# Optimization experiments

Hardware: AMD Instinct MI355X
Metric: run time of the kernel (lower is better)

## Reference

```python
import jax, jax.numpy as jnp
import numpy as np

N, E, D, S, H, L = 20000, 320000, 128, 16, 4, 64


def _ln(x, g, b):
    m = x.mean(-1, keepdims=True)
    v = jnp.mean((x - m) ** 2, -1, keepdims=True)
    return (x - m) / jnp.sqrt(v + 1e-6) * g + b


def _mlp3(x, w1, b1, g1, be1, w2, b2, g2, be2, w3, b3):
    h = jax.nn.silu(_ln(x @ w1 + b1, g1, be1))
    h = jax.nn.silu(_ln(h @ w2 + b2, g2, be2))
    return h @ w3 + b3


def _seg_softmax(a, idx, n):
    # torch_geometric.utils.softmax: per-destination-group stable softmax
    m = jax.ops.segment_max(a, idx, num_segments=n)
    m = jnp.where(jnp.isfinite(m), m, 0.0)
    e = jnp.exp(a - m[idx])
    s = jax.ops.segment_sum(e, idx, num_segments=n)
    return e / (s[idx] + 1e-16)


def setup_inputs() -> dict:
    key = jax.random.key(0)
    ks = jax.random.split(key, 32)
    rn = lambda k, sh, sc=1.0: jax.random.normal(k, sh, dtype=jnp.float32) * sc
    li = lambda k, fi, fo: rn(k, (fi, fo), 1.0 / np.sqrt(fi))
    z = lambda n_: jnp.zeros((n_,), jnp.float32)
    o = lambda n_: jnp.ones((n_,), jnp.float32)
    inp = {
        'node_in': rn(ks[0], (N, D)),
        'node_embed': rn(ks[1], (N, D)),
        'edge_sh': rn(ks[2], (E, S)),
        'edge_length_embedding': rn(ks[3], (E, L)),
        'edge_src': jax.random.randint(ks[4], (E,), 0, N, dtype=jnp.int32),
        'edge_dst': jax.random.randint(ks[5], (E,), 0, N, dtype=jnp.int32),
        'batch': jnp.zeros((N,), jnp.int32),
        'pre_lin_w': li(ks[6], 2 * D + L, D),
        'tp2_w1': li(ks[7], L, 64), 'tp2_b1': z(64),
        'tp2_w2': li(ks[8], 64, H * S), 'tp2_b2': z(H * S),
        'a_w1': li(ks[9], L, 64), 'a_b1': z(64), 'a_g1': o(64), 'a_be1': z(64),
        'a_w2': li(ks[10], 64, 64), 'a_b2': z(64), 'a_g2': o(64), 'a_be2': z(64),
        'a_w3': li(ks[11], 64, H), 'a_b3': z(H),
        'lin_w': li(ks[12], D * H, D),
        'lin_edge_w': li(ks[13], D * H, 64),
        's_w1': li(ks[14], 64, 64), 's_b1': z(64), 's_g1': o(64), 's_be1': z(64),
        's_w2': li(ks[15], 64, 64), 's_b2': z(64), 's_g2': o(64), 's_be2': z(64),
        's_w3': li(ks[16], 64, 32), 's_b3': z(32),
    }
    return inp


def reference(node_in, node_embed, edge_sh, edge_length_embedding, edge_src, edge_dst, batch,
              pre_lin_w, tp2_w1, tp2_b1, tp2_w2, tp2_b2,
              a_w1, a_b1, a_g1, a_be1, a_w2, a_b2, a_g2, a_be2, a_w3, a_b3,
              lin_w, lin_edge_w,
              s_w1, s_b1, s_g1, s_be1, s_w2, s_b2, s_g2, s_be2, s_w3, s_b3):
    e = edge_length_embedding.shape[0]
    n = node_in.shape[0]
    # gather + pre_lin
    msg = jnp.concatenate([node_in[edge_src], node_in[edge_dst], edge_length_embedding], -1) @ pre_lin_w  # [E,D]
    # EquiConv tp2: channelwise TP with radial-MLP per-edge per-(head,sh) weights
    radial = jax.nn.silu(edge_length_embedding @ tp2_w1 + tp2_b1) @ tp2_w2 + tp2_b2  # [E,H*S]
    scal = jnp.einsum('ehs,es->eh', radial.reshape(e, H, S), edge_sh)  # [E,H]
    value = msg[:, None, :] * scal[:, :, None]  # [E,H,D]
    alpha = _mlp3(edge_length_embedding, a_w1, a_b1, a_g1, a_be1, a_w2, a_b2, a_g2, a_be2, a_w3, a_b3)  # [E,H]
    edge_out = value * alpha[:, :, None]  # [E,H,D]
    edge_scalar = _mlp3(edge_out.reshape(e, -1) @ lin_edge_w,
                        s_w1, s_b1, s_g1, s_be1, s_w2, s_b2, s_g2, s_be2, s_w3, s_b3)  # [E,32]
    asm = _seg_softmax(alpha, edge_dst, n)  # [E,H]
    node_fea = jax.ops.segment_sum(value * asm[:, :, None], edge_dst, num_segments=n)  # [N,H,D]
    node_out = node_fea.reshape(n, -1) @ lin_w  # [N,D]
    return node_out, edge_scalar
```

## Files before the change

### kernel.cpp

```cpp
#include <hip/hip_runtime.h>

#define NN 20000
#define EE 320000
#define WTOT 27648

typedef unsigned short u16;
typedef unsigned int u32;
typedef __attribute__((ext_vector_type(8))) short bf16x8;
typedef __attribute__((ext_vector_type(8))) _Float16 f16x8;
typedef __attribute__((ext_vector_type(4))) float f32x4;

__device__ __forceinline__ float bf2f(u16 u){
  union { u32 i; float f; } v; v.i = ((u32)u) << 16; return v.f;
}
__device__ __forceinline__ u16 f2bf(float f){
  union { float f; u32 i; } v; v.f = f;
  u32 i = v.i;
  return (u16)((i + 0x7FFFu + ((i >> 16) & 1u)) >> 16);
}
__device__ __forceinline__ u32 pack2(float a, float b){
  return ((u32)f2bf(b) << 16) | (u32)f2bf(a);
}
__device__ __forceinline__ u16 f2h(float f){
  union { _Float16 h[2]; u32 u; } v; v.h[0] = (_Float16)f;
  return (u16)(v.u & 0xFFFF);
}

__global__ __launch_bounds__(256) void k_prep(
    const float* __restrict__ plw, const float* __restrict__ lew,
    const float* __restrict__ lw,
    u16* __restrict__ Bt1, u16* __restrict__ Bt2, u16* __restrict__ Bt3)
{
  int i = blockIdx.x * 256 + threadIdx.x;
  if (i < 128*320) {
    int n = i / 320, k = i % 320;
    Bt1[i] = f2bf(plw[k*128 + n]);
  }
  int j = i - 128*320;
  if (j >= 0 && j < 256*128) {
    int n = j / 128, k = j % 128;
    int h = n >> 6, c = n & 63;
    Bt2[j] = f2bf(lew[(h*128 + k)*64 + c]);
  }
  int l = i - 128*320 - 256*128;
  if (l >= 0 && l < 128*512) {
    int n = l / 512, k = l % 512;
    Bt3[l] = f2bf(lw[k*128 + n]);
  }
}

__global__ __launch_bounds__(256) void k_prep2(
    const float* __restrict__ aw1, const float* __restrict__ aw2, const float* __restrict__ aw3,
    const float* __restrict__ rw1, const float* __restrict__ rw2,
    const float* __restrict__ sw1, const float* __restrict__ sw2, const float* __restrict__ sw3,
    u16* __restrict__ W)
{
  int i = blockIdx.x * 256 + threadIdx.x;
  if (i >= WTOT) return;
  float v = 0.f;
  int j = i;
  if (j < 8192)      { int n = j >> 6, k = j & 63;
                       v = (n < 64) ? aw1[k*64 + n] : rw1[k*64 + (n - 64)]; }
  else if ((j -= 8192) < 4096) { int n = j >> 6, k = j & 63; v = aw2[k*64 + n]; }
  else if ((j -= 4096) < 1024) { int n = j >> 6, k = j & 63; v = (n < 4) ? aw3[k*4 + n] : 0.f; }
  else if ((j -= 1024) < 4096) { int n = j >> 6, k = j & 63; v = rw2[k*64 + n]; }
  else if ((j -= 4096) < 4096) { int n = j >> 6, k = j & 63; v = sw1[k*64 + n]; }
  else if ((j -= 4096) < 4096) { int n = j >> 6, k = j & 63; v = sw2[k*64 + n]; }
  else               { j -= 4096; int n = j >> 6, k = j & 63; v = sw3[k*32 + n]; }
  W[i] = f2h(v);
}

__global__ __launch_bounds__(256) void k_zero(int* __restrict__ counts){
  int i = blockIdx.x * 256 + threadIdx.x;
  if (i < NN) counts[i] = 0;
}
__global__ __launch_bounds__(256) void k_count(const int* __restrict__ edst, int* __restrict__ counts){
  int e = blockIdx.x * 256 + threadIdx.x;
  if (e < EE) atomicAdd(&counts[edst[e]], 1);
}
__global__ __launch_bounds__(1024) void k_scan(const int* __restrict__ counts,
                                               int* __restrict__ offs, int* __restrict__ cursor){
  __shared__ int part[1024];
  int t = threadIdx.x;
  int c0 = t * 20, c1 = c0 + 20; if (c1 > NN) c1 = NN; if (c0 > NN) c0 = NN;
  int s = 0;
  for (int i = c0; i < c1; ++i) s += counts[i];
  part[t] = s;
  __syncthreads();
  if (t == 0) {
    int run = 0;
    for (int i = 0; i < 1024; ++i) { int v = part[i]; part[i] = run; run += v; }
    offs[NN] = run;
  }
  __syncthreads();
  int run = part[t];
  for (int i = c0; i < c1; ++i) { offs[i] = run; cursor[i] = run; run += counts[i]; }
}
__global__ __launch_bounds__(256) void k_fill(const int* __restrict__ edst,
                                              int* __restrict__ cursor, int* __restrict__ eids){
  int e = blockIdx.x * 256 + threadIdx.x;
  if (e < EE) { int p = atomicAdd(&cursor[edst[e]], 1); eids[p] = e; }
}
__global__ __launch_bounds__(256) void k_sort(const int* __restrict__ offs, int* __restrict__ eids){
  int n = blockIdx.x * 256 + threadIdx.x;
  if (n >= NN) return;
  int b = offs[n], e = offs[n+1];
  for (int i = b + 1; i < e; ++i) {
    int v = eids[i]; int j = i - 1;
    while (j >= b && eids[j] > v) { eids[j+1] = eids[j]; --j; }
    eids[j+1] = v;
  }
}

template<int NI>
__device__ __forceinline__ void gemm16_lds(const u16 (*X)[72], int wrow, int lane,
                                           const u16* __restrict__ B, f32x4 acc[2][4])
{
  const int fr = lane & 15, fc = lane >> 4;
  #pragma unroll
  for (int mi = 0; mi < 2; ++mi)
    #pragma unroll
    for (int ni = 0; ni < NI; ++ni)
      acc[mi][ni] = (f32x4){0.f, 0.f, 0.f, 0.f};
  #pragma unroll
  for (int kk = 0; kk < 2; ++kk) {
    f16x8 a0 = *(const f16x8*)&X[wrow + fr][kk*32 + fc*8];
    f16x8 a1 = *(const f16x8*)&X[wrow + 16 + fr][kk*32 + fc*8];
    #pragma unroll
    for (int ni = 0; ni < NI; ++ni) {
      f16x8 b = *(const f16x8*)(B + (size_t)(ni*16 + fr)*64 + kk*32 + fc*8);
      acc[0][ni] = __builtin_amdgcn_mfma_f32_16x16x32_f16(a0, b, acc[0][ni], 0, 0, 0);
      acc[1][ni] = __builtin_amdgcn_mfma_f32_16x16x32_f16(a1, b, acc[1][ni], 0, 0, 0);
    }
  }
}

template<int NI>
__device__ __forceinline__ void gemm16_lds1(const u16 (*X)[72], int wrow, int lane,
                                            const u16* __restrict__ B, f32x4 acc[4])
{
  const int fr = lane & 15, fc = lane >> 4;
  #pragma unroll
  for (int ni = 0; ni < NI; ++ni) acc[ni] = (f32x4){0.f, 0.f, 0.f, 0.f};
  #pragma unroll
  for (int kk = 0; kk < 2; ++kk) {
    f16x8 a = *(const f16x8*)&X[wrow + fr][kk*32 + fc*8];
    #pragma unroll
    for (int ni = 0; ni < NI; ++ni) {
      f16x8 b = *(const f16x8*)(B + (size_t)(ni*16 + fr)*64 + kk*32 + fc*8);
      acc[ni] = __builtin_amdgcn_mfma_f32_16x16x32_f16(a, b, acc[ni], 0, 0, 0);
    }
  }
}

__device__ __forceinline__ void gemm32_glb8(const float* __restrict__ X, int row0, int lane,
                                            const u16* __restrict__ B, f32x4 acc[2][8])
{
  const int fr = lane & 15, fc = lane >> 4;
  #pragma unroll
  for (int mi = 0; mi < 2; ++mi)
    #pragma unroll
    for (int ni = 0; ni < 8; ++ni)
      acc[mi][ni] = (f32x4){0.f, 0.f, 0.f, 0.f};
  #pragma unroll
  for (int kk = 0; kk < 2; ++kk) {
    const float* p0 = X + (size_t)(row0 + fr)*64 + kk*32 + fc*8;
    const float* p1 = X + (size_t)(row0 + 16 + fr)*64 + kk*32 + fc*8;
    float4 v00 = ((const float4*)p0)[0], v01 = ((const float4*)p0)[1];
    float4 v10 = ((const float4*)p1)[0], v11 = ((const float4*)p1)[1];
    f16x8 a0, a1;
    a0[0]=(_Float16)v00.x; a0[1]=(_Float16)v00.y; a0[2]=(_Float16)v00.z; a0[3]=(_Float16)v00.w;
    a0[4]=(_Float16)v01.x; a0[5]=(_Float16)v01.y; a0[6]=(_Float16)v01.z; a0[7]=(_Float16)v01.w;
    a1[0]=(_Float16)v10.x; a1[1]=(_Float16)v10.y; a1[2]=(_Float16)v10.z; a1[3]=(_Float16)v10.w;
    a1[4]=(_Float16)v11.x; a1[5]=(_Float16)v11.y; a1[6]=(_Float16)v11.z; a1[7]=(_Float16)v11.w;
    #pragma unroll
    for (int ni = 0; ni < 8; ++ni) {
      f16x8 b = *(const f16x8*)(B + (size_t)(ni*16 + fr)*64 + kk*32 + fc*8);
      acc[0][ni] = __builtin_amdgcn_mfma_f32_16x16x32_f16(a0, b, acc[0][ni], 0, 0, 0);
      acc[1][ni] = __builtin_amdgcn_mfma_f32_16x16x32_f16(a1, b, acc[1][ni], 0, 0, 0);
    }
  }
}

template<bool LN>
__device__ __forceinline__ void act_store16(f32x4 acc[2][4],
    const float* __restrict__ b, const float* __restrict__ g, const float* __restrict__ be,
    u16 (*H)[72], int wrow, int lane)
{
  const int fr = lane & 15, fc = lane >> 4;
  float bv[4], gv[4], bev[4];
  #pragma unroll
  for (int ni = 0; ni < 4; ++ni) {
    bv[ni] = b[ni*16 + fr];
    if (LN) { gv[ni] = g[ni*16 + fr]; bev[ni] = be[ni*16 + fr]; }
  }
  #pragma unroll
  for (int mi = 0; mi < 2; ++mi)
    #pragma unroll
    for (int j = 0; j < 4; ++j) {
      int r = wrow + mi*16 + fc*4 + j;
      float x[4];
      #pragma unroll
      for (int ni = 0; ni < 4; ++ni) x[ni] = acc[mi][ni][j] + bv[ni];
      if (LN) {
        float s  = x[0] + x[1] + x[2] + x[3];
        float s2 = x[0]*x[0] + x[1]*x[1] + x[2]*x[2] + x[3]*x[3];
        #pragma unroll
        for (int off = 1; off < 16; off <<= 1) {
          s  += __shfl_xor(s,  off);
          s2 += __shfl_xor(s2, off);
        }
        float mu  = s * (1.f/64.f);
        float var = s2 * (1.f/64.f) - mu*mu;
        float rs  = rsqrtf(var + 1e-6f);
        #pragma unroll
        for (int ni = 0; ni < 4; ++ni) x[ni] = (x[ni] - mu)*rs*gv[ni] + bev[ni];
      }
      #pragma unroll
      for (int ni = 0; ni < 4; ++ni) {
        float y = x[ni];
        y = y / (1.f + __expf(-y));
        H[r][ni*16 + fr] = f2h(y);
      }
    }
}

template<bool LN>
__device__ __forceinline__ void act_store16_1(f32x4 acc[4],
    const float* __restrict__ b, const float* __restrict__ g, const float* __restrict__ be,
    u16 (*H)[72], int wrow, int lane)
{
  const int fr = lane & 15, fc = lane >> 4;
  float bv[4], gv[4], bev[4];
  #pragma unroll
  for (int ni = 0; ni < 4; ++ni) {
    bv[ni] = b[ni*16 + fr];
    if (LN) { gv[ni] = g[ni*16 + fr]; bev[ni] = be[ni*16 + fr]; }
  }
  #pragma unroll
  for (int j = 0; j < 4; ++j) {
    int r = wrow + fc*4 + j;
    float x[4];
    #pragma unroll
    for (int ni = 0; ni < 4; ++ni) x[ni] = acc[ni][j] + bv[ni];
    if (LN) {
      float s  = x[0] + x[1] + x[2] + x[3];
      float s2 = x[0]*x[0] + x[1]*x[1] + x[2]*x[2] + x[3]*x[3];
      #pragma unroll
      for (int off = 1; off < 16; off <<= 1) {
        s  += __shfl_xor(s,  off);
        s2 += __shfl_xor(s2, off);
      }
      float mu  = s * (1.f/64.f);
      float var = s2 * (1.f/64.f) - mu*mu;
      float rs  = rsqrtf(var + 1e-6f);
      #pragma unroll
      for (int ni = 0; ni < 4; ++ni) x[ni] = (x[ni] - mu)*rs*gv[ni] + bev[ni];
    }
    #pragma unroll
    for (int ni = 0; ni < 4; ++ni) {
      float y = x[ni];
      y = y / (1.f + __expf(-y));
      H[r][ni*16 + fr] = f2h(y);
    }
  }
}

__global__ __launch_bounds__(256, 4) void k_ar_mlp(
  const float* __restrict__ elen,
  const float* __restrict__ esh, const u16* __restrict__ Wm,
  const float* __restrict__ ab1, const float* __restrict__ ag1, const float* __restrict__ abe1,
  const float* __restrict__ ab2, const float* __restrict__ ag2, const float* __restrict__ abe2,
  const float* __restrict__ ab3,
  const float* __restrict__ tb1, const float* __restrict__ tb2,
  float* __restrict__ alpha_g, float* __restrict__ scal_g, float* __restrict__ cbuf_g)
{
  __shared__ u16 Ha[128][72], Hr[128][72];
  __shared__ float aS[128][4];
  const u16* Wc1 = Wm;
  const u16* Wa2 = Wm + 8192;
  const u16* Wa3 = Wm + 12288;
  const u16* Wr2 = Wm + 13312;
  const int tid = threadIdx.x;
  const int wave = tid >> 6, lane = tid & 63;
  const int fr = lane & 15, fc = lane >> 4;
  const int wrow = wave * 32;
  const int e0 = blockIdx.x * 128;
  {
    f32x4 acc8[2][8];
    gemm32_glb8(elen, e0 + wrow, lane, Wc1, acc8);
    float bva[4], gva[4], beva[4], bvr[4];
    #pragma unroll
    for (int ni = 0; ni < 4; ++ni) {
      bva[ni] = ab1[ni*16 + fr]; gva[ni] = ag1[ni*16 + fr]; beva[ni] = abe1[ni*16 + fr];
      bvr[ni] = tb1[ni*16 + fr];
    }
    #pragma unroll
    for (int mi = 0; mi < 2; ++mi)
      #pragma unroll
      for (int j = 0; j < 4; ++j) {
        int r = wrow + mi*16 + fc*4 + j;
        float xa[4], xr[4];
        #pragma unroll
        for (int ni = 0; ni < 4; ++ni) {
          xa[ni] = acc8[mi][ni][j] + bva[ni];
          xr[ni] = acc8[mi][ni+4][j] + bvr[ni];
        }
        float s  = xa[0] + xa[1] + xa[2] + xa[3];
        float s2 = xa[0]*xa[0] + xa[1]*xa[1] + xa[2]*xa[2] + xa[3]*xa[3];
        #pragma unroll
        for (int off = 1; off < 16; off <<= 1) {
          s  += __shfl_xor(s,  off);
          s2 += __shfl_xor(s2, off);
        }
        float mu  = s * (1.f/64.f);
        float var = s2 * (1.f/64.f) - mu*mu;
        float rs  = rsqrtf(var + 1e-6f);
        #pragma unroll
        for (int ni = 0; ni < 4; ++ni) {
          float y = (xa[ni] - mu)*rs*gva[ni] + beva[ni];
          y = y / (1.f + __expf(-y));
          Ha[r][ni*16 + fr] = f2h(y);
          float z = xr[ni];
          z = z / (1.f + __expf(-z));
          Hr[r][ni*16 + fr] = f2h(z);
        }
      }
  }
  f32x4 acc[2][4];
  gemm16_lds<4>(Ha, wrow, lane, Wa2, acc);
  act_store16<true>(acc, ab2, ag2, abe2, Ha, wrow, lane);
  gemm16_lds<1>(Ha, wrow, lane, Wa3, acc);
  {
    float bv = (fr < 4) ? ab3[fr] : 0.f;
    #pragma unroll
    for (int mi = 0; mi < 2; ++mi)
      #pragma unroll
      for (int j = 0; j < 4; ++j) {
        int r = wrow + mi*16 + fc*4 + j;
        float v = acc[mi][0][j] + bv;
        if (fr < 4) {
          alpha_g[(size_t)(e0 + r)*4 + fr] = v;
          aS[r][fr] = v;
        }
      }
  }
  gemm16_lds<4>(Hr, wrow, lane, Wr2, acc);
  {
    float bv[4];
    #pragma unroll
    for (int ni = 0; ni < 4; ++ni) bv[ni] = tb2[ni*16 + fr];
    #pragma unroll
    for (int mi = 0; mi < 2; ++mi)
      #pragma unroll
      for (int j = 0; j < 4; ++j) {
        int r = wrow + mi*16 + fc*4 + j;
        float shv = esh[(size_t)(e0 + r)*16 + fr];
        float sc[4];
        #pragma unroll
        for (int ni = 0; ni < 4; ++ni) {
          float t = (acc[mi][ni][j] + bv[ni]) * shv;
          #pragma unroll
          for (int off = 1; off < 16; off <<= 1) t += __shfl_xor(t, off);
          sc[ni] = t;
        }
        if (fr == 0) {
          float4 sv; sv.x = sc[0]; sv.y = sc[1]; sv.z = sc[2]; sv.w = sc[3];
          *(float4*)(scal_g + (size_t)(e0 + r)*4) = sv;
          float4 cv;
          cv.x = sc[0]*aS[r][0]; cv.y = sc[1]*aS[r][1];
          cv.z = sc[2]*aS[r][2]; cv.w = sc[3]*aS[r][3];
          *(float4*)(cbuf_g + (size_t)(e0 + r)*4) = cv;
        }
      }
  }
}

__global__ __launch_bounds__(256) void g1_msg(
    const float* __restrict__ node_in, const float* __restrict__ elen,
    const int* __restrict__ esrc, const int* __restrict__ edst,
    const u16* __restrict__ Bt1, u16* __restrict__ msgb)
{
  __shared__ u16 As[128][40];
  __shared__ u16 Bs[128][40];
  const int tid = threadIdx.x;
  const int e0 = blockIdx.x * 128;
  const int wave = tid >> 6, lane = tid & 63;
  const int wr = (wave >> 1) * 64, wc = (wave & 1) * 64;
  const int fr = lane & 15, fc = lane >> 4;
  f32x4 acc[4][4] = {};
  const int r = tid >> 1, half = tid & 1;
  const int e = e0 + r;
  const int s_idx = esrc[e], d_idx = edst[e];
  for (int k0 = 0; k0 < 320; k0 += 32) {
    const int kk = k0 + half * 16;
    const float* ap;
    if (kk < 128)      ap = node_in + (size_t)s_idx*128 + kk;
    else if (kk < 256) ap = node_in + (size_t)d_idx*128 + (kk - 128);
    else               ap = elen + (size_t)e*64 + (kk - 256);
    u32* asp = (u32*)&As[r][half*16];
    #pragma unroll
    for (int q = 0; q < 4; ++q) {
      float4 v = *(const float4*)(ap + q*4);
      asp[q*2]   = pack2(v.x, v.y);
      asp[q*2+1] = pack2(v.z, v.w);
    }
    const uint4* bp = (const uint4*)(Bt1 + (size_t)r*320 + kk);
    *(uint4*)&Bs[r][half*16]     = bp[0];
    *(uint4*)&Bs[r][half*16 + 8] = bp[1];
    __syncthreads();
    bf16x8 a[4], b[4];
    #pragma unroll
    for (int mi = 0; mi < 4; ++mi) a[mi] = *(const bf16x8*)&As[wr + mi*16 + fr][fc*8];
    #pragma unroll
    for (int ni = 0; ni < 4; ++ni) b[ni] = *(const bf16x8*)&Bs[wc + ni*16 + fr][fc*8];
    #pragma unroll
    for (int mi = 0; mi < 4; ++mi)
      #pragma unroll
      for (int ni = 0; ni < 4; ++ni)
        acc[mi][ni] = __builtin_amdgcn_mfma_f32_16x16x32_bf16(a[mi], b[ni], acc[mi][ni], 0, 0, 0);
    __syncthreads();
  }
  #pragma unroll
  for (int mi = 0; mi < 4; ++mi)
    #pragma unroll
    for (int j = 0; j < 4; ++j) {
      int row = wr + mi*16 + fc*4 + j;
      size_t base = (size_t)(e0 + row)*128 + wc + fr;
      #pragma unroll
      for (int ni = 0; ni < 4; ++ni)
        msgb[base + ni*16] = f2bf(acc[mi][ni][j]);
    }
}

union G2Smem {
  struct { u16 As[64][40]; u16 Bs[256][40]; } s;
  u16 X[64][72];
};
__global__ __launch_bounds__(256, 4) void g2s(
    const u16* __restrict__ msgb, const u16* __restrict__ Bt2,
    const float* __restrict__ cbuf, const u16* __restrict__ Wm,
    const float* __restrict__ b1, const float* __restrict__ g1, const float* __restrict__ be1,
    const float* __restrict__ b2, const float* __restrict__ g2, const float* __restrict__ be2,
    const float* __restrict__ b3,
    float* __restrict__ oute)
{
  __shared__ G2Smem u;
  __shared__ float cS[64][4];
  const u16* Ws1 = Wm + 17408;
  const u16* Ws2 = Wm + 21504;
  const u16* Ws3 = Wm + 25600;
  const int tid = threadIdx.x, wave = tid >> 6, lane = tid & 63;
  const int e0 = blockIdx.x * 64;
  const int fr = lane & 15, fc = lane >> 4;
  const int wrow = wave * 16;
  cS[tid >> 2][tid & 3] = cbuf[(size_t)e0*4 + tid];
  f32x4 acc[16];
  #pragma unroll
  for (int ni = 0; ni < 16; ++ni) acc[ni] = (f32x4){0.f, 0.f, 0.f, 0.f};
  for (int k0 = 0; k0 < 128; k0 += 32) {
    {
      int r = tid >> 2, q = tid & 3;
      *(uint4*)&u.s.As[r][q*8] = *(const uint4*)(msgb + (size_t)(e0 + r)*128 + k0 + q*8);
    }
    {
      const uint4* bp = (const uint4*)(Bt2 + (size_t)tid*128 + k0);
      *(uint4*)&u.s.Bs[tid][0]  = bp[0];
      *(uint4*)&u.s.Bs[tid][8]  = bp[1];
      *(uint4*)&u.s.Bs[tid][16] = bp[2];
      *(uint4*)&u.s.Bs[tid][24] = bp[3];
    }
    __syncthreads();
    bf16x8 a = *(const bf16x8*)&u.s.As[wrow + fr][fc*8];
    #pragma unroll
    for (int ni = 0; ni < 16; ++ni) {
      bf16x8 b = *(const bf16x8*)&u.s.Bs[ni*16 + fr][fc*8];
      acc[ni] = __builtin_amdgcn_mfma_f32_16x16x32_bf16(a, b, acc[ni], 0, 0, 0);
    }
    __syncthreads();
  }
  #pragma unroll
  for (int j = 0; j < 4; ++j) {
    int r = wrow + fc*4 + j;
    float c0 = cS[r][0], c1 = cS[r][1], c2 = cS[r][2], c3 = cS[r][3];
    #pragma unroll
    for (int m = 0; m < 4; ++m) {
      float y = c0*acc[m][j] + c1*acc[4+m][j] + c2*acc[8+m][j] + c3*acc[12+m][j];
      u.X[r][m*16 + fr] = f2h(y);
    }
  }
  f32x4 sa[4];
  gemm16_lds1<4>(u.X, wrow, lane, Ws1, sa);
  act_store16_1<true>(sa, b1, g1, be1, u.X, wrow, lane);
  gemm16_lds1<4>(u.X, wrow, lane, Ws2, sa);
  act_store16_1<true>(sa, b2, g2, be2, u.X, wrow, lane);
  gemm16_lds1<2>(u.X, wrow, lane, Ws3, sa);
  {
    float bv[2];
    bv[0] = b3[fr]; bv[1] = b3[16 + fr];
    #pragma unroll
    for (int j = 0; j < 4; ++j) {
      int r = wrow + fc*4 + j;
      #pragma unroll
      for (int ni = 0; ni < 2; ++ni)
        oute[(size_t)(e0 + r)*32 + ni*16 + fr] = sa[ni][j] + bv[ni];
    }
  }
}

__global__ __launch_bounds__(256) void k_node(
  const int* __restrict__ offs, const int* __restrict__ eids,
  const float* __restrict__ alpha, const float* __restrict__ scal,
  const u16* __restrict__ msgb, u16* __restrict__ nfb)
{
  const int w = threadIdx.x >> 6, lane = threadIdx.x & 63;
  const int n = blockIdx.x * 4 + w;
  const int beg = offs[n], end = offs[n+1];
  float m0=-3e38f, m1=-3e38f, m2=-3e38f, m3=-3e38f;
  for (int i = beg + lane; i < end; i += 64) {
    int eid = eids[i];
    float4 a = *(const float4*)(alpha + (size_t)eid*4);
    m0 = fmaxf(m0, a.x); m1 = fmaxf(m1, a.y);
    m2 = fmaxf(m2, a.z); m3 = fmaxf(m3, a.w);
  }
  #pragma unroll
  for (int off = 1; off < 64; off <<= 1) {
    m0 = fmaxf(m0, __shfl_xor(m0, off));
    m1 = fmaxf(m1, __shfl_xor(m1, off));
    m2 = fmaxf(m2, __shfl_xor(m2, off));
    m3 = fmaxf(m3, __shfl_xor(m3, off));
  }
  float se0=0.f, se1=0.f, se2=0.f, se3=0.f;
  float f00=0.f, f01=0.f, f10=0.f, f11=0.f, f20=0.f, f21=0.f, f30=0.f, f31=0.f;
  for (int i = beg; i < end; ++i) {
    int eid = eids[i];
    float4 a = *(const float4*)(alpha + (size_t)eid*4);
    float4 s = *(const float4*)(scal + (size_t)eid*4);
    float e0 = __expf(a.x - m0), e1 = __expf(a.y - m1);
    float e2 = __expf(a.z - m2), e3 = __expf(a.w - m3);
    se0 += e0; se1 += e1; se2 += e2; se3 += e3;
    float w0 = e0*s.x, w1 = e1*s.y, w2 = e2*s.z, w3 = e3*s.w;
    float v0 = bf2f(msgb[(size_t)eid*128 + lane]);
    float v1 = bf2f(msgb[(size_t)eid*128 + 64 + lane]);
    f00 = fmaf(w0, v0, f00); f01 = fmaf(w0, v1, f01);
    f10 = fmaf(w1, v0, f10); f11 = fmaf(w1, v1, f11);
    f20 = fmaf(w2, v0, f20); f21 = fmaf(w2, v1, f21);
    f30 = fmaf(w3, v0, f30); f31 = fmaf(w3, v1, f31);
  }
  float i0 = 1.f/(se0 + 1e-16f), i1 = 1.f/(se1 + 1e-16f);
  float i2 = 1.f/(se2 + 1e-16f), i3 = 1.f/(se3 + 1e-16f);
  size_t b = (size_t)n * 512;
  nfb[b + 0*128 + lane]      = f2bf(f00*i0);
  nfb[b + 0*128 + 64 + lane] = f2bf(f01*i0);
  nfb[b + 1*128 + lane]      = f2bf(f10*i1);
  nfb[b + 1*128 + 64 + lane] = f2bf(f11*i1);
  nfb[b + 2*128 + lane]      = f2bf(f20*i2);
  nfb[b + 2*128 + 64 + lane] = f2bf(f21*i2);
  nfb[b + 3*128 + lane]      = f2bf(f30*i3);
  nfb[b + 3*128 + 64 + lane] = f2bf(f31*i3);
}

__global__ __launch_bounds__(256) void g10_out(
    const u16* __restrict__ nfb, const u16* __restrict__ Bt3,
    float* __restrict__ out)
{
  __shared__ u16 As[128][40];
  __shared__ u16 Bs[128][40];
  const int tid = threadIdx.x;
  const int n0 = blockIdx.x * 128;
  const int wave = tid >> 6, lane = tid & 63;
  const int wr = (wave >> 1) * 64, wc = (wave & 1) * 64;
  const int fr = lane & 15, fc = lane >> 4;
  f32x4 acc[4][4] = {};
  const int r = tid >> 1, half = tid & 1;
  const int n = n0 + r;
  for (int k0 = 0; k0 < 512; k0 += 32) {
    uint4 z; z.x=0; z.y=0; z.z=0; z.w=0;
    uint4 v0 = z, v1 = z;
    if (n < NN) {
      const uint4* apv = (const uint4*)(nfb + (size_t)n*512 + k0 + half*16);
      v0 = apv[0]; v1 = apv[1];
    }
    *(uint4*)&As[r][half*16]     = v0;
    *(uint4*)&As[r][half*16 + 8] = v1;
    const uint4* bp = (const uint4*)(Bt3 + (size_t)r*512 + k0 + half*16);
    *(uint4*)&Bs[r][half*16]     = bp[0];
    *(uint4*)&Bs[r][half*16 + 8] = bp[1];
    __syncthreads();
    bf16x8 a[4], b[4];
    #pragma unroll
    for (int mi = 0; mi < 4; ++mi) a[mi] = *(const bf16x8*)&As[wr + mi*16 + fr][fc*8];
    #pragma unroll
    for (int ni = 0; ni < 4; ++ni) b[ni] = *(const bf16x8*)&Bs[wc + ni*16 + fr][fc*8];
    #pragma unroll
    for (int mi = 0; mi < 4; ++mi)
      #pragma unroll
      for (int ni = 0; ni < 4; ++ni)
        acc[mi][ni] = __builtin_amdgcn_mfma_f32_16x16x32_bf16(a[mi], b[ni], acc[mi][ni], 0, 0, 0);
    __syncthreads();
  }
  #pragma unroll
  for (int mi = 0; mi < 4; ++mi)
    #pragma unroll
    for (int j = 0; j < 4; ++j) {
      int rowg = n0 + wr + mi*16 + fc*4 + j;
      if (rowg < NN) {
        size_t base = (size_t)rowg*128 + wc + fr;
        #pragma unroll
        for (int ni = 0; ni < 4; ++ni)
          out[base + ni*16] = acc[mi][ni][j];
      }
    }
}

extern "C" void kernel_launch(void* const* d_in, const int* in_sizes, int n_in,
                              void* d_out, int out_size, void* d_ws, size_t ws_size,
                              hipStream_t stream)
{
  const float* node_in    = (const float*)d_in[0];
  const float* edge_sh    = (const float*)d_in[2];
  const float* elen       = (const float*)d_in[3];
  const int*   esrc       = (const int*)d_in[4];
  const int*   edst       = (const int*)d_in[5];
  const float* pre_lin_w  = (const float*)d_in[7];
  const float* tp2_w1     = (const float*)d_in[8];
  const float* tp2_b1     = (const float*)d_in[9];
  const float* tp2_w2     = (const float*)d_in[10];
  const float* tp2_b2     = (const float*)d_in[11];
  const float* a_w1  = (const float*)d_in[12];
  const float* a_b1  = (const float*)d_in[13];
  const float* a_g1  = (const float*)d_in[14];
  const float* a_be1 = (const float*)d_in[15];
  const float* a_w2  = (const float*)d_in[16];
  const float* a_b2  = (const float*)d_in[17];
  const float* a_g2  = (const float*)d_in[18];
  const float* a_be2 = (const float*)d_in[19];
  const float* a_w3  = (const float*)d_in[20];
  const float* a_b3  = (const float*)d_in[21];
  const float* lin_w      = (const float*)d_in[22];
  const float* lin_edge_w = (const float*)d_in[23];
  const float* s_w1  = (const float*)d_in[24];
  const float* s_b1  = (const float*)d_in[25];
  const float* s_g1  = (const float*)d_in[26];
  const float* s_be1 = (const float*)d_in[27];
  const float* s_w2  = (const float*)d_in[28];
  const float* s_b2  = (const float*)d_in[29];
  const float* s_g2  = (const float*)d_in[30];
  const float* s_be2 = (const float*)d_in[31];
  const float* s_w3  = (const float*)d_in[32];
  const float* s_b3  = (const float*)d_in[33];

  float* out_node = (float*)d_out;
  float* out_edge = out_node + (size_t)NN * 128;

  char* ws = (char*)d_ws;
  size_t off = 0;
  auto take = [&](size_t bytes) -> char* {
    char* p = ws + off;
    off = (off + bytes + 255) & ~(size_t)255;
    return p;
  };
  u16*   msgb   = (u16*)take((size_t)EE * 128 * 2);
  u16*   nfb    = (u16*)take((size_t)NN * 512 * 2);
  float* alpha  = (float*)take((size_t)EE * 4 * 4);
  float* scal   = (float*)take((size_t)EE * 4 * 4);
  float* cbuf   = (float*)take((size_t)EE * 4 * 4);
  int*   counts = (int*)take((size_t)NN * 4);
  int*   offs   = (int*)take((size_t)(NN + 1) * 4);
  int*   cursor = (int*)take((size_t)NN * 4);
  int*   eids   = (int*)take((size_t)EE * 4);
  u16*   Bt1    = (u16*)take((size_t)128 * 320 * 2);
  u16*   Bt2    = (u16*)take((size_t)256 * 128 * 2);
  u16*   Bt3    = (u16*)take((size_t)128 * 512 * 2);
  u16*   Wmlp   = (u16*)take((size_t)WTOT * 2);

  k_prep<<<544, 256, 0, stream>>>(pre_lin_w, lin_edge_w, lin_w, Bt1, Bt2, Bt3);
  k_prep2<<<(WTOT + 255)/256, 256, 0, stream>>>(a_w1, a_w2, a_w3, tp2_w1, tp2_w2,
                                                s_w1, s_w2, s_w3, Wmlp);
  k_zero<<<(NN + 255)/256, 256, 0, stream>>>(counts);
  k_count<<<EE/256, 256, 0, stream>>>(edst, counts);
  k_scan<<<1, 1024, 0, stream>>>(counts, offs, cursor);
  k_fill<<<EE/256, 256, 0, stream>>>(edst, cursor, eids);
  k_sort<<<(NN + 255)/256, 256, 0, stream>>>(offs, eids);
  k_ar_mlp<<<EE/128, 256, 0, stream>>>(elen, edge_sh, Wmlp,
                                       a_b1, a_g1, a_be1, a_b2, a_g2, a_be2, a_b3,
                                       tp2_b1, tp2_b2, alpha, scal, cbuf);
  g1_msg<<<EE/128, 256, 0, stream>>>(node_in, elen, esrc, edst, Bt1, msgb);
  g2s<<<EE/64, 256, 0, stream>>>(msgb, Bt2, cbuf, Wmlp,
                                 s_b1, s_g1, s_be1, s_b2, s_g2, s_be2, s_b3, out_edge);
  k_node<<<NN/4, 256, 0, stream>>>(offs, eids, alpha, scal, msgb, nfb);
  g10_out<<<(NN + 127)/128, 256, 0, stream>>>(nfb, Bt3, out_node);
}
```

Measured before the change: 467.2 us.

## Double-buffer g2s LDS tiles with XOR swizzle to overlap loads and MFMA

```diff
diff --git a/kernel.cpp b/kernel.cpp
--- a/kernel.cpp
+++ b/kernel.cpp
@@ -25,6 +25,7 @@
   union { _Float16 h[2]; u32 u; } v; v.h[0] = (_Float16)f;
   return (u16)(v.u & 0xFFFF);
 }
+__device__ __forceinline__ int sw4(int r){ return ((r >> 2) ^ (r >> 4)) & 3; }
 
 __global__ __launch_bounds__(256) void k_prep(
     const float* __restrict__ plw, const float* __restrict__ lew,
@@ -434,10 +435,10 @@
 }
 
 union G2Smem {
-  struct { u16 As[64][40]; u16 Bs[256][40]; } s;
+  struct { u16 As[2][64][40]; u16 Bs[2][256][40]; } s;
   u16 X[64][72];
 };
-__global__ __launch_bounds__(256, 4) void g2s(
+__global__ __launch_bounds__(256, 3) void g2s(
     const u16* __restrict__ msgb, const u16* __restrict__ Bt2,
     const float* __restrict__ cbuf, const u16* __restrict__ Wm,
     const float* __restrict__ b1, const float* __restrict__ g1, const float* __restrict__ be1,
@@ -455,27 +456,44 @@
   const int fr = lane & 15, fc = lane >> 4;
   const int wrow = wave * 16;
   cS[tid >> 2][tid & 3] = cbuf[(size_t)e0*4 + tid];
+  const int ar = tid >> 2, aq = tid & 3;
+  const int asw = (aq ^ sw4(ar)) * 8;
+  const int bsw0 = (0 ^ sw4(tid)) * 8, bsw1 = (1 ^ sw4(tid)) * 8;
+  const int bsw2 = (2 ^ sw4(tid)) * 8, bsw3 = (3 ^ sw4(tid)) * 8;
+  const u16* asrc = msgb + (size_t)(e0 + ar)*128 + aq*8;
+  const u16* bsrc = Bt2 + (size_t)tid*128;
+  const int arow = wrow + fr;
+  const int acol = (fc ^ sw4(arow)) * 8;
   f32x4 acc[16];
   #pragma unroll
   for (int ni = 0; ni < 16; ++ni) acc[ni] = (f32x4){0.f, 0.f, 0.f, 0.f};
-  for (int k0 = 0; k0 < 128; k0 += 32) {
-    {
-      int r = tid >> 2, q = tid & 3;
-      *(uint4*)&u.s.As[r][q*8] = *(const uint4*)(msgb + (size_t)(e0 + r)*128 + k0 + q*8);
-    }
-    {
-      const uint4* bp = (const uint4*)(Bt2 + (size_t)tid*128 + k0);
-      *(uint4*)&u.s.Bs[tid][0]  = bp[0];
-      *(uint4*)&u.s.Bs[tid][8]  = bp[1];
-      *(uint4*)&u.s.Bs[tid][16] = bp[2];
-      *(uint4*)&u.s.Bs[tid][24] = bp[3];
-    }
-    __syncthreads();
-    bf16x8 a = *(const bf16x8*)&u.s.As[wrow + fr][fc*8];
+  *(uint4*)&u.s.As[0][ar][asw] = *(const uint4*)(asrc);
+  {
+    const uint4* bp = (const uint4*)(bsrc);
+    *(uint4*)&u.s.Bs[0][tid][bsw0] = bp[0];
+    *(uint4*)&u.s.Bs[0][tid][bsw1] = bp[1];
+    *(uint4*)&u.s.Bs[0][tid][bsw2] = bp[2];
+    *(uint4*)&u.s.Bs[0][tid][bsw3] = bp[3];
+  }
+  __syncthreads();
+  #pragma unroll
+  for (int k0i = 0; k0i < 4; ++k0i) {
+    const int cur = k0i & 1;
+    bf16x8 a = *(const bf16x8*)&u.s.As[cur][arow][acol];
     #pragma unroll
     for (int ni = 0; ni < 16; ++ni) {
-      bf16x8 b = *(const bf16x8*)&u.s.Bs[ni*16 + fr][fc*8];
+      int row = ni*16 + fr;
+      bf16x8 b = *(const bf16x8*)&u.s.Bs[cur][row][(fc ^ sw4(row))*8];
       acc[ni] = __builtin_amdgcn_mfma_f32_16x16x32_bf16(a, b, acc[ni], 0, 0, 0);
+    }
+    if (k0i < 3) {
+      const int k1 = (k0i + 1) * 32;
+      *(uint4*)&u.s.As[cur^1][ar][asw] = *(const uint4*)(asrc + k1);
+      const uint4* bp = (const uint4*)(bsrc + k1);
+      *(uint4*)&u.s.Bs[cur^1][tid][bsw0] = bp[0];
+      *(uint4*)&u.s.Bs[cur^1][tid][bsw1] = bp[1];
+      *(uint4*)&u.s.Bs[cur^1][tid][bsw2] = bp[2];
+      *(uint4*)&u.s.Bs[cur^1][tid][bsw3] = bp[3];
     }
     __syncthreads();
   }
```

New measurement: 471.5 us. Within noise of the previous version (+0.9%).
